# Kernel optimization log

Measured on AMD Instinct MI355X. Metric: run time of the kernel, lower is better.

The kernel has to match this reference:

```python
import jax, jax.numpy as jnp
import numpy as np
import math

N_FREQ = 128
D_EMB = 64
SLOT_DIM = 256
MLP_HIDDEN = 1024
B, N_SLOTS, N_FEAT = 32, 128, 4096
SIN_DIM = 1 + 2 * N_FREQ
EPS_LN = 1e-5


def _lin_init(key, dout, din):
    k1, k2 = jax.random.split(key)
    s = 1.0 / np.sqrt(din)
    w = jax.random.uniform(k1, (dout, din), minval=-s, maxval=s, dtype=jnp.float32)
    b = jax.random.uniform(k2, (dout,), minval=-s, maxval=s, dtype=jnp.float32)
    return w, b


def setup_inputs() -> dict:
    key = jax.random.key(0)
    ks = jax.random.split(key, 20)
    inp = {}
    # four TimeDepWeight heads: (prefix, d_out, d_in)
    heads = [("q", SLOT_DIM, SLOT_DIM), ("g", SLOT_DIM, 2 * SLOT_DIM),
             ("f0", MLP_HIDDEN, 2 * SLOT_DIM), ("f1", SLOT_DIM, MLP_HIDDEN)]
    i = 0
    for name, dout, din in heads:
        w0, b0 = _lin_init(ks[i], D_EMB, SIN_DIM)
        w1, b1 = _lin_init(ks[i + 1], D_EMB, D_EMB)
        wp, bp = _lin_init(ks[i + 2], dout * din, D_EMB)
        i += 3
        inp[f"{name}_w0"], inp[f"{name}_b0"] = w0, b0
        inp[f"{name}_w1"], inp[f"{name}_b1"] = w1, b1
        inp[f"{name}_wp"], inp[f"{name}_bp"] = wp, bp
    # LayerNorm affine params (eqx.nn.LayerNorm defaults: weight=1, bias=0)
    inp["lnA_w"] = jnp.ones((SLOT_DIM,), jnp.float32)
    inp["lnA_b"] = jnp.zeros((SLOT_DIM,), jnp.float32)
    inp["lnF_w"] = jnp.ones((SLOT_DIM,), jnp.float32)
    inp["lnF_b"] = jnp.zeros((SLOT_DIM,), jnp.float32)
    inp["t"] = jax.random.uniform(ks[12], (1,), dtype=jnp.float32)
    inp["slots"] = jax.random.normal(ks[13], (B, N_SLOTS, SLOT_DIM), jnp.float32)
    inp["k"] = jax.random.normal(ks[14], (B, N_FEAT, SLOT_DIM), jnp.float32)
    inp["v"] = jax.random.normal(ks[15], (B, N_FEAT, SLOT_DIM), jnp.float32)
    return inp


def _tdw(t, w0, b0, w1, b1, wp, bp, d_out, d_in):
    # Sinusoidal(t) -> 2-layer SiLU MLP -> proj -> [d_out, d_in]
    freqs = (-math.log(10000.0) / N_FREQ) * jnp.arange(N_FREQ, dtype=jnp.float32)
    wt = freqs * t
    emb = jnp.concatenate([t[None], jnp.sin(wt), jnp.cos(wt)])
    h = jax.nn.silu(w0 @ emb + b0)
    h = jax.nn.silu(w1 @ h + b1)
    return (wp @ h + bp).reshape(d_out, d_in)


def _layernorm(x, w, b):
    mu = x.mean(-1, keepdims=True)
    var = ((x - mu) ** 2).mean(-1, keepdims=True)
    return (x - mu) / jnp.sqrt(var + EPS_LN) * w + b


def reference(t, slots, k, v,
              q_w0, q_b0, q_w1, q_b1, q_wp, q_bp,
              g_w0, g_b0, g_w1, g_b1, g_wp, g_bp,
              f0_w0, f0_b0, f0_w1, f0_b1, f0_wp, f0_bp,
              f1_w0, f1_b0, f1_w1, f1_b1, f1_wp, f1_bp,
              lnA_w, lnA_b, lnF_w, lnF_b):
    ts = t[0]
    scale = SLOT_DIM ** (-0.5)
    W_q = _tdw(ts, q_w0, q_b0, q_w1, q_b1, q_wp, q_bp, SLOT_DIM, SLOT_DIM)
    W_gate = _tdw(ts, g_w0, g_b0, g_w1, g_b1, g_wp, g_bp, SLOT_DIM, 2 * SLOT_DIM)
    W_ff0 = _tdw(ts, f0_w0, f0_b0, f0_w1, f0_b1, f0_wp, f0_bp, MLP_HIDDEN, 2 * SLOT_DIM)
    W_ff1 = _tdw(ts, f1_w0, f1_b0, f1_w1, f1_b1, f1_wp, f1_bp, SLOT_DIM, MLP_HIDDEN)

    slots_norm = _layernorm(slots, lnA_w, lnA_b)                  # [B,N,D]
    q = jnp.einsum('bnd,od->bno', slots_norm, W_q)                # [B,N,D]
    att_logits = jnp.einsum('bnd,bmd->bnm', q, k) * scale         # [B,N,M]
    att = jax.nn.softmax(att_logits, axis=1)                      # over slots
    att = att / (att.sum(axis=-1, keepdims=True) + 1e-08)         # renorm over feats
    f_attn = jnp.einsum('bnm,bmd->bnd', att, v)                   # [B,N,D]

    gate_input = jnp.concatenate([slots_norm, f_attn], axis=-1)   # [B,N,2D]
    gate = jax.nn.sigmoid(jnp.einsum('bnd,od->bno', gate_input, W_gate))

    slots_ff = _layernorm(slots, lnF_w, lnF_b)
    ff_input = jnp.concatenate([slots_ff, f_attn], axis=-1)       # [B,N,2D]
    h = jax.nn.relu(jnp.einsum('bnd,od->bno', ff_input, W_ff0))   # [B,N,H]
    g_ff = jnp.einsum('bnd,od->bno', h, W_ff1)                    # [B,N,D]
    return gate * f_attn + g_ff
```

## Files before the change

### kernel.cpp

```cpp
#include <hip/hip_runtime.h>
#include <hip/hip_bf16.h>
#include <cstdint>

typedef unsigned short u16;
typedef unsigned int u32;
typedef __attribute__((ext_vector_type(8))) short short8;
typedef __attribute__((ext_vector_type(4))) float f32x4;

#define TID ((int)threadIdx.x)

__device__ __forceinline__ float b2f(u16 u) { return __uint_as_float(((u32)u) << 16); }
__device__ __forceinline__ u16 f2b(float f) {
    u32 u = __float_as_uint(f);
    u += 0x7fffu + ((u >> 16) & 1u);
    return (u16)(u >> 16);
}
__device__ __forceinline__ float2 upk(u32 u) {
    float2 r;
    r.x = __uint_as_float(u << 16);
    r.y = __uint_as_float(u & 0xffff0000u);
    return r;
}
__device__ __forceinline__ float silu_f(float x) { return x / (1.f + __expf(-x)); }

__device__ __forceinline__ float ldx(const void* p, size_t i, bool bf) {
    float v;
    if (bf) v = b2f(((const u16*)p)[i]);
    else    v = ((const float*)p)[i];
    return v;
}

#define BB 32
#define NN 128
#define DD 256
#define MM 4096
#define HH 1024
#define BN (BB * NN)

#define O_FLAG 0
#define O_H2   8
#define O_S    (O_H2 + 256)
#define O_FAT  (O_S + BN)
#define O_WQT  (O_FAT + BN * DD)
#define O_WGT  (O_WQT + 256 * 256)
#define O_WF0T (O_WGT + 512 * 256)
#define O_WF1T (O_WF0T + 512 * 1024)
#define O_SNA  (O_WF1T + 1024 * 256)
#define O_SNF  (O_SNA + BN * DD)
#define O_Q    (O_SNF + BN * DD)
#define O_H    (O_Q + BN * DD)
#define O_FATP O_H

__global__ void probe_dtype(const void* lnAw, int* flag) {
    u32 bits = *(const u32*)lnAw;
    *flag = ((bits & 0xFFFFu) == 0x3F80u) ? 1 : 0;
}

__global__ __launch_bounds__(256) void tdw_mlp(
    const void* t,
    const void* qw0, const void* qb0, const void* qw1, const void* qb1,
    const void* gw0, const void* gb0, const void* gw1, const void* gb1,
    const void* f0w0, const void* f0b0, const void* f0w1, const void* f0b1,
    const void* f1w0, const void* f1b0, const void* f1w1, const void* f1b1,
    float* h2out, const int* flagp)
{
    __shared__ float emb[257];
    __shared__ float h1s[256];
    bool bf = (*flagp != 0);
    float tv = ldx(t, 0, bf);
    const float c = -9.210340371976184f / 128.f;
    for (int i = TID; i < 257; i += 256) {
        float val;
        if (i == 0) val = tv;
        else if (i <= 128) val = sinf(c * (float)(i - 1) * tv);
        else val = cosf(c * (float)(i - 129) * tv);
        emb[i] = val;
    }
    __syncthreads();
    int head = TID >> 6, o = TID & 63;
    const void* w0s[4] = {qw0, gw0, f0w0, f1w0};
    const void* b0s[4] = {qb0, gb0, f0b0, f1b0};
    const void* w1s[4] = {qw1, gw1, f0w1, f1w1};
    const void* b1s[4] = {qb1, gb1, f0b1, f1b1};
    float acc = ldx(b0s[head], o, bf);
    if (bf) {
        const u16* w0 = (const u16*)w0s[head];
        for (int j = 0; j < 257; j++) acc += b2f(w0[o * 257 + j]) * emb[j];
    } else {
        const float* w0 = (const float*)w0s[head];
        for (int j = 0; j < 257; j++) acc += w0[o * 257 + j] * emb[j];
    }
    h1s[TID] = silu_f(acc);
    __syncthreads();
    float acc2 = ldx(b1s[head], o, bf);
    if (bf) {
        const u16* w1 = (const u16*)w1s[head];
        for (int j = 0; j < 64; j++) acc2 += b2f(w1[o * 64 + j]) * h1s[head * 64 + j];
    } else {
        const float* w1 = (const float*)w1s[head];
        for (int j = 0; j < 64; j++) acc2 += w1[o * 64 + j] * h1s[head * 64 + j];
    }
    h2out[TID] = silu_f(acc2);
}

__global__ __launch_bounds__(256) void tdw_proj(
    const void* __restrict__ wp, const void* __restrict__ bp,
    const float* __restrict__ h2, float* __restrict__ WT,
    int dout_shift, int din, const int* flagp)
{
    __shared__ float h2s[64];
    bool bf = (*flagp != 0);
    if (TID < 64) h2s[TID] = h2[TID];
    __syncthreads();
    int j = blockIdx.x * 256 + TID;
    int d = j >> dout_shift;
    int o = j & ((1 << dout_shift) - 1);
    long i = (long)o * din + d;
    float acc;
    if (bf) acc = b2f(((const u16*)bp)[i]);
    else    acc = ((const float*)bp)[i];
    if (bf) {
        const uint4* row = (const uint4*)((const u16*)wp + i * 64);
#pragma unroll
        for (int r = 0; r < 8; r++) {
            uint4 u = row[r];
            float2 p;
            p = upk(u.x); acc += p.x * h2s[r * 8 + 0] + p.y * h2s[r * 8 + 1];
            p = upk(u.y); acc += p.x * h2s[r * 8 + 2] + p.y * h2s[r * 8 + 3];
            p = upk(u.z); acc += p.x * h2s[r * 8 + 4] + p.y * h2s[r * 8 + 5];
            p = upk(u.w); acc += p.x * h2s[r * 8 + 6] + p.y * h2s[r * 8 + 7];
        }
    } else {
        const float4* row = (const float4*)((const float*)wp + i * 64);
#pragma unroll
        for (int r = 0; r < 16; r++) {
            float4 u = row[r];
            acc += u.x * h2s[r * 4 + 0] + u.y * h2s[r * 4 + 1]
                 + u.z * h2s[r * 4 + 2] + u.w * h2s[r * 4 + 3];
        }
    }
    WT[j] = acc;
}

__global__ __launch_bounds__(256) void layernorm_k(
    const void* __restrict__ slots,
    const void* lnAw, const void* lnAb, const void* lnFw, const void* lnFb,
    float* __restrict__ snA, float* __restrict__ snF, const int* flagp)
{
    int bn = blockIdx.x;
    bool bf = (*flagp != 0);
    float x;
    if (bf) x = b2f(((const u16*)slots)[(size_t)bn * DD + TID]);
    else    x = ((const float*)slots)[(size_t)bn * DD + TID];
    float s1 = x, s2 = x * x;
    for (int off = 32; off; off >>= 1) {
        s1 += __shfl_down(s1, off, 64);
        s2 += __shfl_down(s2, off, 64);
    }
    __shared__ float r1[4], r2[4];
    __shared__ float mu_s, rs_s;
    if ((TID & 63) == 0) { r1[TID >> 6] = s1; r2[TID >> 6] = s2; }
    __syncthreads();
    if (TID == 0) {
        float a = r1[0] + r1[1] + r1[2] + r1[3];
        float b = r2[0] + r2[1] + r2[2] + r2[3];
        float mu = a * (1.f / 256.f);
        float var = b * (1.f / 256.f) - mu * mu;
        mu_s = mu;
        rs_s = rsqrtf(var + 1e-5f);
    }
    __syncthreads();
    float xh = (x - mu_s) * rs_s;
    snA[(size_t)bn * DD + TID] = xh * ldx(lnAw, TID, bf) + ldx(lnAb, TID, bf);
    snF[(size_t)bn * DD + TID] = xh * ldx(lnFw, TID, bf) + ldx(lnFb, TID, bf);
}

__global__ __launch_bounds__(256) void qproj(
    const float* __restrict__ snA, const float* __restrict__ WqT, u16* __restrict__ qb)
{
    int rb = blockIdx.x;
    __shared__ float sn[8][256];
    for (int idx = TID; idx < 512; idx += 256) {
        int r = idx >> 6, q4 = idx & 63;
        *(float4*)&sn[r][q4 * 4] = *(const float4*)(snA + (size_t)rb * 2048 + r * 256 + q4 * 4);
    }
    __syncthreads();
    float acc[8] = {0, 0, 0, 0, 0, 0, 0, 0};
    for (int d = 0; d < 256; d += 4) {
        float w0 = WqT[(d + 0) * 256 + TID];
        float w1 = WqT[(d + 1) * 256 + TID];
        float w2 = WqT[(d + 2) * 256 + TID];
        float w3 = WqT[(d + 3) * 256 + TID];
#pragma unroll
        for (int r = 0; r < 8; r++) {
            float4 s4 = *(const float4*)&sn[r][d];
            acc[r] = fmaf(s4.x, w0, fmaf(s4.y, w1, fmaf(s4.z, w2, fmaf(s4.w, w3, acc[r]))));
        }
    }
    for (int r = 0; r < 8; r++) qb[(size_t)(rb * 8 + r) * 256 + TID] = f2b(acc[r]);
}

__global__ __launch_bounds__(256, 2) void attn_mfma(
    const u16* __restrict__ qbG,
    const void* __restrict__ k, const void* __restrict__ v,
    float* __restrict__ fatP, float* __restrict__ S, const int* flagp)
{
    const int b = blockIdx.y;
    const int mt = blockIdx.x;
    const int m0 = mt * 128;
    const bool bf = (*flagp != 0);
    const int t = TID;
    const int l = t & 63, w = t >> 6;
    const int lg = l >> 4;
    const int ll = l & 15;

    __shared__ alignas(16) u16 AB[128 * 128];
    __shared__ alignas(16) u16 vt[256 * 40];

    u16* qb = AB;
    u16* kb = AB + 8192;

    f32x4 acc[2][8];
#pragma unroll
    for (int s = 0; s < 2; s++)
#pragma unroll
        for (int nt = 0; nt < 8; nt++) acc[s][nt] = {0.f, 0.f, 0.f, 0.f};

    for (int dc = 0; dc < 4; dc++) {
        {
            const u32* qg = (const u32*)qbG + (size_t)b * 128 * 128 + dc * 32;
#pragma unroll
            for (int i = 0; i < 16; i++) {
                int fid = i * 256 + t;
                int n = fid >> 5, dp = fid & 31;
                u32 val = qg[n * 128 + dp];
                *(u32*)((char*)qb + n * 128 + ((dp * 4) ^ ((n & 7) << 4))) = val;
            }
        }
        if (bf) {
            const u32* kg = (const u32*)k + ((size_t)(b * MM + m0)) * 128 + dc * 32;
#pragma unroll
            for (int i = 0; i < 16; i++) {
                int fid = i * 256 + t;
                int mm = fid >> 5, dp = fid & 31;
                u32 val = kg[(size_t)mm * 128 + dp];
                *(u32*)((char*)kb + mm * 128 + ((dp * 4) ^ ((mm & 7) << 4))) = val;
            }
        } else {
            const float4* kg = (const float4*)k + ((size_t)(b * MM + m0)) * 64 + dc * 16;
#pragma unroll
            for (int i = 0; i < 8; i++) {
                int fid = i * 256 + t;
                int mm = fid >> 4, q4 = fid & 15;
                float4 f = kg[(size_t)mm * 64 + q4];
                u32 p0 = ((u32)f2b(f.x)) | ((u32)f2b(f.y) << 16);
                u32 p1 = ((u32)f2b(f.z)) | ((u32)f2b(f.w) << 16);
                char* base = (char*)kb + mm * 128;
                *(u32*)(base + (((q4 * 8) + 0) ^ ((mm & 7) << 4))) = p0;
                *(u32*)(base + (((q4 * 8) + 4) ^ ((mm & 7) << 4))) = p1;
            }
        }
        __syncthreads();
#pragma unroll
        for (int ds = 0; ds < 2; ds++) {
            int doff = ds * 64 + lg * 16;
            short8 bfr[2];
#pragma unroll
            for (int s = 0; s < 2; s++) {
                int mm = w * 32 + s * 16 + ll;
                bfr[s] = *(const short8*)((char*)kb + mm * 128 + (doff ^ ((mm & 7) << 4)));
            }
#pragma unroll
            for (int nt = 0; nt < 8; nt++) {
                int n = nt * 16 + ll;
                short8 af = *(const short8*)((char*)qb + n * 128 + (doff ^ ((n & 7) << 4)));
                acc[0][nt] = __builtin_amdgcn_mfma_f32_16x16x32_bf16(af, bfr[0], acc[0][nt], 0, 0, 0);
                acc[1][nt] = __builtin_amdgcn_mfma_f32_16x16x32_bf16(af, bfr[1], acc[1][nt], 0, 0, 0);
            }
        }
        __syncthreads();
    }

    const float scale = 0.0625f;
#pragma unroll
    for (int s = 0; s < 2; s++) {
        float cm = -1e30f;
#pragma unroll
        for (int nt = 0; nt < 8; nt++)
#pragma unroll
            for (int r = 0; r < 4; r++) cm = fmaxf(cm, acc[s][nt][r]);
        cm = fmaxf(cm, __shfl_xor(cm, 16));
        cm = fmaxf(cm, __shfl_xor(cm, 32));
        float cs = 0.f;
#pragma unroll
        for (int nt = 0; nt < 8; nt++)
#pragma unroll
            for (int r = 0; r < 4; r++) {
                float ev = __expf((acc[s][nt][r] - cm) * scale);
                acc[s][nt][r] = ev;
                cs += ev;
            }
        cs += __shfl_xor(cs, 16);
        cs += __shfl_xor(cs, 32);
        float inv = 1.f / cs;
#pragma unroll
        for (int nt = 0; nt < 8; nt++)
#pragma unroll
            for (int r = 0; r < 4; r++) acc[s][nt][r] *= inv;
    }

    u16* att = AB;
#pragma unroll
    for (int s = 0; s < 2; s++)
#pragma unroll
        for (int nt = 0; nt < 8; nt++)
#pragma unroll
            for (int r = 0; r < 4; r++) {
                int n = nt * 16 + lg * 4 + r;
                int mw = w * 32 + s * 16 + ll;
                *(u16*)((char*)att + n * 256 + ((mw * 2) ^ ((n & 7) << 4))) = f2b(acc[s][nt][r]);
            }
#pragma unroll
    for (int nt = 0; nt < 8; nt++)
#pragma unroll
        for (int r = 0; r < 4; r++) {
            float vsum = acc[0][nt][r] + acc[1][nt][r];
            vsum += __shfl_xor(vsum, 1);
            vsum += __shfl_xor(vsum, 2);
            vsum += __shfl_xor(vsum, 4);
            vsum += __shfl_xor(vsum, 8);
            if (ll == 0) atomicAdd(S + b * NN + nt * 16 + lg * 4 + r, vsum);
        }

    f32x4 accp[8][4];
#pragma unroll
    for (int nt = 0; nt < 8; nt++)
#pragma unroll
        for (int dt = 0; dt < 4; dt++) accp[nt][dt] = {0.f, 0.f, 0.f, 0.f};

    for (int ms = 0; ms < 4; ms++) {
        if (bf) {
            const u32* vg = (const u32*)v + ((size_t)(b * MM + m0 + ms * 32)) * 128;
#pragma unroll
            for (int i = 0; i < 16; i++) {
                int fid = i * 256 + t;
                int mm = fid >> 7, du = fid & 127;
                u32 val = vg[(size_t)mm * 128 + du];
                vt[(du * 2 + 0) * 40 + mm] = (u16)(val & 0xffffu);
                vt[(du * 2 + 1) * 40 + mm] = (u16)(val >> 16);
            }
        } else {
            const float4* vg = (const float4*)v + ((size_t)(b * MM + m0 + ms * 32)) * 64;
#pragma unroll
            for (int i = 0; i < 8; i++) {
                int fid = i * 256 + t;
                int mm = fid >> 6, q4 = fid & 63;
                float4 f = vg[(size_t)mm * 64 + q4];
                vt[(q4 * 4 + 0) * 40 + mm] = f2b(f.x);
                vt[(q4 * 4 + 1) * 40 + mm] = f2b(f.y);
                vt[(q4 * 4 + 2) * 40 + mm] = f2b(f.z);
                vt[(q4 * 4 + 3) * 40 + mm] = f2b(f.w);
            }
        }
        __syncthreads();
        short8 bfr[4];
#pragma unroll
        for (int dt = 0; dt < 4; dt++) {
            int dv = w * 64 + dt * 16 + ll;
            bfr[dt] = *(const short8*)(vt + dv * 40 + lg * 8);
        }
#pragma unroll
        for (int nt = 0; nt < 8; nt++) {
            int n = nt * 16 + ll;
            short8 af = *(const short8*)((char*)att + n * 256 + ((ms * 64 + lg * 16) ^ ((n & 7) << 4)));
#pragma unroll
            for (int dt = 0; dt < 4; dt++)
                accp[nt][dt] = __builtin_amdgcn_mfma_f32_16x16x32_bf16(af, bfr[dt], accp[nt][dt], 0, 0, 0);
        }
        __syncthreads();
    }

    float* fp = fatP + ((size_t)mt * BN + (size_t)b * NN) * DD;
#pragma unroll
    for (int nt = 0; nt < 8; nt++)
#pragma unroll
        for (int dt = 0; dt < 4; dt++)
#pragma unroll
            for (int r = 0; r < 4; r++) {
                int n = nt * 16 + lg * 4 + r;
                int dv = w * 64 + dt * 16 + ll;
                fp[(size_t)n * DD + dv] = accp[nt][dt][r];
            }
}

__global__ __launch_bounds__(256) void reduce_fat(
    const float* __restrict__ fatP, float* __restrict__ fat)
{
    size_t i = ((size_t)blockIdx.x * 256 + TID) * 4;
    float4 a = *(const float4*)(fatP + i);
#pragma unroll
    for (int mt = 1; mt < 32; mt++) {
        float4 bb = *(const float4*)(fatP + (size_t)mt * (size_t)BN * DD + i);
        a.x += bb.x; a.y += bb.y; a.z += bb.z; a.w += bb.w;
    }
    *(float4*)(fat + i) = a;
}

__global__ __launch_bounds__(256) void ffa(
    const float* __restrict__ snF, const float* __restrict__ fat, const float* __restrict__ S,
    const float* __restrict__ Wf0T, float* __restrict__ h)
{
    int rb = blockIdx.x;
    __shared__ float fi[8][512];
    __shared__ float rsh[8];
    if (TID < 8) rsh[TID] = 1.f / (S[rb * 8 + TID] + 1e-8f);
    __syncthreads();
    for (int idx = TID; idx < 1024; idx += 256) {
        int r = idx >> 7, q4 = idx & 127;
        size_t bn = (size_t)rb * 8 + r;
        float4 val;
        if (q4 < 64) val = *(const float4*)(snF + bn * 256 + q4 * 4);
        else {
            val = *(const float4*)(fat + bn * 256 + (q4 - 64) * 4);
            float s = rsh[r];
            val.x *= s; val.y *= s; val.z *= s; val.w *= s;
        }
        *(float4*)&fi[r][q4 * 4] = val;
    }
    __syncthreads();
    float acc[8][4] = {};
    for (int d = 0; d < 512; d += 4) {
        float w[4][4];
#pragma unroll
        for (int kk2 = 0; kk2 < 4; kk2++) {
            const float* wp_ = Wf0T + (size_t)(d + kk2) * 1024 + TID;
            w[kk2][0] = wp_[0];   w[kk2][1] = wp_[256];
            w[kk2][2] = wp_[512]; w[kk2][3] = wp_[768];
        }
#pragma unroll
        for (int r = 0; r < 8; r++) {
            float4 f = *(const float4*)&fi[r][d];
            float fv[4] = {f.x, f.y, f.z, f.w};
#pragma unroll
            for (int kk2 = 0; kk2 < 4; kk2++)
#pragma unroll
                for (int c = 0; c < 4; c++)
                    acc[r][c] = fmaf(fv[kk2], w[kk2][c], acc[r][c]);
        }
    }
    for (int r = 0; r < 8; r++) {
        size_t base = (size_t)(rb * 8 + r) * 1024;
        h[base + TID] = fmaxf(acc[r][0], 0.f);
        h[base + TID + 256] = fmaxf(acc[r][1], 0.f);
        h[base + TID + 512] = fmaxf(acc[r][2], 0.f);
        h[base + TID + 768] = fmaxf(acc[r][3], 0.f);
    }
}

__global__ __launch_bounds__(256) void ffb(
    const float* __restrict__ snA, const float* __restrict__ fat, const float* __restrict__ S,
    const float* __restrict__ WgT, const float* __restrict__ Wf1T,
    const float* __restrict__ h, void* __restrict__ out, const int* flagp)
{
    int rb = blockIdx.x;
    bool bf = (*flagp != 0);
    __shared__ float gi[8][512];
    __shared__ float hs[8][1024];
    __shared__ float rsh[8];
    if (TID < 8) rsh[TID] = 1.f / (S[rb * 8 + TID] + 1e-8f);
    __syncthreads();
    for (int idx = TID; idx < 1024; idx += 256) {
        int r = idx >> 7, q4 = idx & 127;
        size_t bn = (size_t)rb * 8 + r;
        float4 val;
        if (q4 < 64) val = *(const float4*)(snA + bn * 256 + q4 * 4);
        else {
            val = *(const float4*)(fat + bn * 256 + (q4 - 64) * 4);
            float s = rsh[r];
            val.x *= s; val.y *= s; val.z *= s; val.w *= s;
        }
        *(float4*)&gi[r][q4 * 4] = val;
    }
    for (int idx = TID; idx < 2048; idx += 256) {
        int r = idx >> 8, q4 = idx & 255;
        *(float4*)&hs[r][q4 * 4] = *(const float4*)(h + (size_t)(rb * 8 + r) * 1024 + q4 * 4);
    }
    __syncthreads();
    float ag[8] = {0, 0, 0, 0, 0, 0, 0, 0};
    float af[8] = {0, 0, 0, 0, 0, 0, 0, 0};
    for (int d = 0; d < 512; d += 4) {
        float w0 = WgT[(d + 0) * 256 + TID];
        float w1 = WgT[(d + 1) * 256 + TID];
        float w2 = WgT[(d + 2) * 256 + TID];
        float w3 = WgT[(d + 3) * 256 + TID];
#pragma unroll
        for (int r = 0; r < 8; r++) {
            float4 g = *(const float4*)&gi[r][d];
            ag[r] = fmaf(g.x, w0, fmaf(g.y, w1, fmaf(g.z, w2, fmaf(g.w, w3, ag[r]))));
        }
    }
    for (int j = 0; j < 1024; j += 4) {
        float w0 = Wf1T[(j + 0) * 256 + TID];
        float w1 = Wf1T[(j + 1) * 256 + TID];
        float w2 = Wf1T[(j + 2) * 256 + TID];
        float w3 = Wf1T[(j + 3) * 256 + TID];
#pragma unroll
        for (int r = 0; r < 8; r++) {
            float4 hv = *(const float4*)&hs[r][j];
            af[r] = fmaf(hv.x, w0, fmaf(hv.y, w1, fmaf(hv.z, w2, fmaf(hv.w, w3, af[r]))));
        }
    }
    for (int r = 0; r < 8; r++) {
        int bn = rb * 8 + r;
        float fa = gi[r][256 + TID];
        float g = 1.f / (1.f + __expf(-ag[r]));
        float val = g * fa + af[r];
        if (bf) ((u16*)out)[(size_t)bn * 256 + TID] = f2b(val);
        else    ((float*)out)[(size_t)bn * 256 + TID] = val;
    }
}

extern "C" void kernel_launch(void* const* d_in, const int* in_sizes, int n_in,
                              void* d_out, int out_size, void* d_ws, size_t ws_size,
                              hipStream_t stream)
{
    const void* in[32];
    bool sig_order = (n_in >= 1 && in_sizes[0] == 1);
    for (int i = 0; i < 32; i++) {
        int j = sig_order ? ((i < 28) ? (i + 4) : (i - 28)) : i;
        in[i] = d_in[j];
    }

    const void* qw0 = in[0];  const void* qb0 = in[1];
    const void* qw1 = in[2];  const void* qb1 = in[3];
    const void* qwp = in[4];  const void* qbp = in[5];
    const void* gw0 = in[6];  const void* gb0 = in[7];
    const void* gw1 = in[8];  const void* gb1 = in[9];
    const void* gwp = in[10]; const void* gbp = in[11];
    const void* f0w0 = in[12]; const void* f0b0 = in[13];
    const void* f0w1 = in[14]; const void* f0b1 = in[15];
    const void* f0wp = in[16]; const void* f0bp = in[17];
    const void* f1w0 = in[18]; const void* f1b0 = in[19];
    const void* f1w1 = in[20]; const void* f1b1 = in[21];
    const void* f1wp = in[22]; const void* f1bp = in[23];
    const void* lnAw = in[24]; const void* lnAb = in[25];
    const void* lnFw = in[26]; const void* lnFb = in[27];
    const void* t    = in[28]; const void* slots = in[29];
    const void* kk   = in[30]; const void* vv   = in[31];

    float* F = (float*)d_ws;
    int* flagp = (int*)(F + O_FLAG);

    hipMemsetAsync(F + O_S, 0, (size_t)BN * sizeof(float), stream);

    probe_dtype<<<1, 1, 0, stream>>>(lnAw, flagp);

    tdw_mlp<<<1, 256, 0, stream>>>(t, qw0, qb0, qw1, qb1, gw0, gb0, gw1, gb1,
                                   f0w0, f0b0, f0w1, f0b1, f1w0, f1b0, f1w1, f1b1,
                                   F + O_H2, flagp);

    tdw_proj<<<256, 256, 0, stream>>>(qwp, qbp, F + O_H2 + 0, F + O_WQT, 8, 256, flagp);
    tdw_proj<<<512, 256, 0, stream>>>(gwp, gbp, F + O_H2 + 64, F + O_WGT, 8, 512, flagp);
    tdw_proj<<<2048, 256, 0, stream>>>(f0wp, f0bp, F + O_H2 + 128, F + O_WF0T, 10, 512, flagp);
    tdw_proj<<<1024, 256, 0, stream>>>(f1wp, f1bp, F + O_H2 + 192, F + O_WF1T, 8, 1024, flagp);

    layernorm_k<<<BN, 256, 0, stream>>>(slots, lnAw, lnAb, lnFw, lnFb,
                                        F + O_SNA, F + O_SNF, flagp);

    qproj<<<BN / 8, 256, 0, stream>>>(F + O_SNA, F + O_WQT, (u16*)(F + O_Q));

    attn_mfma<<<dim3(MM / 128, BB), 256, 0, stream>>>((const u16*)(F + O_Q), kk, vv,
                                                      F + O_FATP, F + O_S, flagp);

    reduce_fat<<<BN * DD / 1024, 256, 0, stream>>>(F + O_FATP, F + O_FAT);

    ffa<<<BN / 8, 256, 0, stream>>>(F + O_SNF, F + O_FAT, F + O_S, F + O_WF0T, F + O_H);

    ffb<<<BN / 8, 256, 0, stream>>>(F + O_SNA, F + O_FAT, F + O_S, F + O_WGT, F + O_WF1T,
                                    F + O_H, d_out, flagp);
}
```

Measured before the change: 1.012 ms.

## Process two feature sub-tiles per attention block and use per-wave staging

Each attention block now covers 256 features in two 128-feature sub-tiles and keeps the att·V accumulator across both, which halves the number of fp32 partial outputs that reduce_fat has to sum. Q fragments are read straight from global memory instead of being staged in shared memory. K and V tiles go into per-wave shared-memory regions, so most block-wide barriers can be dropped. The costs are fewer blocks (less parallelism), uncoalesced strided column loads for V, and repeated global reads of Q.

```diff
diff --git a/kernel.cpp b/kernel.cpp
--- a/kernel.cpp
+++ b/kernel.cpp
@@ -36,6 +36,7 @@
 #define MM 4096
 #define HH 1024
 #define BN (BB * NN)
+#define NMT 16
 
 #define O_FLAG 0
 #define O_H2   8
@@ -207,175 +208,171 @@
 {
     const int b = blockIdx.y;
     const int mt = blockIdx.x;
-    const int m0 = mt * 128;
     const bool bf = (*flagp != 0);
     const int t = TID;
     const int l = t & 63, w = t >> 6;
     const int lg = l >> 4;
     const int ll = l & 15;
 
-    __shared__ alignas(16) u16 AB[128 * 128];
-    __shared__ alignas(16) u16 vt[256 * 40];
-
-    u16* qb = AB;
-    u16* kb = AB + 8192;
-
-    f32x4 acc[2][8];
-#pragma unroll
-    for (int s = 0; s < 2; s++)
-#pragma unroll
-        for (int nt = 0; nt < 8; nt++) acc[s][nt] = {0.f, 0.f, 0.f, 0.f};
-
-    for (int dc = 0; dc < 4; dc++) {
-        {
-            const u32* qg = (const u32*)qbG + (size_t)b * 128 * 128 + dc * 32;
-#pragma unroll
-            for (int i = 0; i < 16; i++) {
-                int fid = i * 256 + t;
-                int n = fid >> 5, dp = fid & 31;
-                u32 val = qg[n * 128 + dp];
-                *(u32*)((char*)qb + n * 128 + ((dp * 4) ^ ((n & 7) << 4))) = val;
-            }
-        }
-        if (bf) {
-            const u32* kg = (const u32*)k + ((size_t)(b * MM + m0)) * 128 + dc * 32;
-#pragma unroll
-            for (int i = 0; i < 16; i++) {
-                int fid = i * 256 + t;
-                int mm = fid >> 5, dp = fid & 31;
-                u32 val = kg[(size_t)mm * 128 + dp];
-                *(u32*)((char*)kb + mm * 128 + ((dp * 4) ^ ((mm & 7) << 4))) = val;
-            }
-        } else {
-            const float4* kg = (const float4*)k + ((size_t)(b * MM + m0)) * 64 + dc * 16;
-#pragma unroll
-            for (int i = 0; i < 8; i++) {
-                int fid = i * 256 + t;
-                int mm = fid >> 4, q4 = fid & 15;
-                float4 f = kg[(size_t)mm * 64 + q4];
-                u32 p0 = ((u32)f2b(f.x)) | ((u32)f2b(f.y) << 16);
-                u32 p1 = ((u32)f2b(f.z)) | ((u32)f2b(f.w) << 16);
-                char* base = (char*)kb + mm * 128;
-                *(u32*)(base + (((q4 * 8) + 0) ^ ((mm & 7) << 4))) = p0;
-                *(u32*)(base + (((q4 * 8) + 4) ^ ((mm & 7) << 4))) = p1;
-            }
-        }
+    __shared__ alignas(16) u16 att[128 * 128];
+    __shared__ alignas(16) u16 vt[4 * 2176];
+
+    char* kb_w = (char*)att + w * 4096;
+    char* vt_w = (char*)vt + w * 4352;
+
+    const u16* qrow = qbG + (size_t)(b * 128) * 256;
+
+    f32x4 accp[8][4];
+#pragma unroll
+    for (int nt = 0; nt < 8; nt++)
+#pragma unroll
+        for (int dt = 0; dt < 4; dt++) accp[nt][dt] = {0.f, 0.f, 0.f, 0.f};
+
+    for (int sub = 0; sub < 2; sub++) {
+        const int msub = mt * 256 + sub * 128;
+
+        f32x4 acc[2][8];
+#pragma unroll
+        for (int s = 0; s < 2; s++)
+#pragma unroll
+            for (int nt = 0; nt < 8; nt++) acc[s][nt] = {0.f, 0.f, 0.f, 0.f};
+
+        for (int dc = 0; dc < 4; dc++) {
+            if (bf) {
+                const u32* kg = (const u32*)k + ((size_t)(b * MM + msub + w * 32)) * 128 + dc * 32;
+#pragma unroll
+                for (int i = 0; i < 16; i++) {
+                    int fid = i * 64 + l;
+                    int dp = fid & 31, lm = fid >> 5;
+                    u32 val = kg[(size_t)lm * 128 + dp];
+                    *(u32*)(kb_w + lm * 128 + ((dp * 4) ^ ((lm & 7) << 4))) = val;
+                }
+            } else {
+                const float2* kg = (const float2*)k + ((size_t)(b * MM + msub + w * 32)) * 128 + dc * 32;
+#pragma unroll
+                for (int i = 0; i < 16; i++) {
+                    int fid = i * 64 + l;
+                    int dp = fid & 31, lm = fid >> 5;
+                    float2 f = kg[(size_t)lm * 128 + dp];
+                    u32 val = (u32)f2b(f.x) | ((u32)f2b(f.y) << 16);
+                    *(u32*)(kb_w + lm * 128 + ((dp * 4) ^ ((lm & 7) << 4))) = val;
+                }
+            }
+            asm volatile("" ::: "memory");
+#pragma unroll
+            for (int ds = 0; ds < 2; ds++) {
+                int doff = ds * 64 + lg * 16;
+                short8 bfr[2];
+#pragma unroll
+                for (int s = 0; s < 2; s++) {
+                    int lm = s * 16 + ll;
+                    bfr[s] = *(const short8*)(kb_w + lm * 128 + (doff ^ ((lm & 7) << 4)));
+                }
+#pragma unroll
+                for (int nt = 0; nt < 8; nt++) {
+                    short8 af = *(const short8*)(qrow + (size_t)(nt * 16 + ll) * 256
+                                                 + dc * 64 + ds * 32 + lg * 8);
+                    acc[0][nt] = __builtin_amdgcn_mfma_f32_16x16x32_bf16(af, bfr[0], acc[0][nt], 0, 0, 0);
+                    acc[1][nt] = __builtin_amdgcn_mfma_f32_16x16x32_bf16(af, bfr[1], acc[1][nt], 0, 0, 0);
+                }
+            }
+            asm volatile("" ::: "memory");
+        }
+
+        const float scale = 0.0625f;
+#pragma unroll
+        for (int s = 0; s < 2; s++) {
+            float cm = -1e30f;
+#pragma unroll
+            for (int nt = 0; nt < 8; nt++)
+#pragma unroll
+                for (int r = 0; r < 4; r++) cm = fmaxf(cm, acc[s][nt][r]);
+            cm = fmaxf(cm, __shfl_xor(cm, 16));
+            cm = fmaxf(cm, __shfl_xor(cm, 32));
+            float cs = 0.f;
+#pragma unroll
+            for (int nt = 0; nt < 8; nt++)
+#pragma unroll
+                for (int r = 0; r < 4; r++) {
+                    float ev = __expf((acc[s][nt][r] - cm) * scale);
+                    acc[s][nt][r] = ev;
+                    cs += ev;
+                }
+            cs += __shfl_xor(cs, 16);
+            cs += __shfl_xor(cs, 32);
+            float inv = 1.f / cs;
+#pragma unroll
+            for (int nt = 0; nt < 8; nt++)
+#pragma unroll
+                for (int r = 0; r < 4; r++) acc[s][nt][r] *= inv;
+        }
+
         __syncthreads();
-#pragma unroll
-        for (int ds = 0; ds < 2; ds++) {
-            int doff = ds * 64 + lg * 16;
-            short8 bfr[2];
-#pragma unroll
-            for (int s = 0; s < 2; s++) {
-                int mm = w * 32 + s * 16 + ll;
-                bfr[s] = *(const short8*)((char*)kb + mm * 128 + (doff ^ ((mm & 7) << 4)));
+
+#pragma unroll
+        for (int s = 0; s < 2; s++)
+#pragma unroll
+            for (int nt = 0; nt < 8; nt++)
+#pragma unroll
+                for (int r = 0; r < 4; r++) {
+                    int n = nt * 16 + lg * 4 + r;
+                    int mw = w * 32 + s * 16 + ll;
+                    *(u16*)((char*)att + n * 256 + ((mw * 2) ^ ((n & 7) << 4))) = f2b(acc[s][nt][r]);
+                }
+#pragma unroll
+        for (int nt = 0; nt < 8; nt++)
+#pragma unroll
+            for (int r = 0; r < 4; r++) {
+                float vsum = acc[0][nt][r] + acc[1][nt][r];
+                vsum += __shfl_xor(vsum, 1);
+                vsum += __shfl_xor(vsum, 2);
+                vsum += __shfl_xor(vsum, 4);
+                vsum += __shfl_xor(vsum, 8);
+                if (ll == 0) atomicAdd(S + b * NN + nt * 16 + lg * 4 + r, vsum);
+            }
+        __syncthreads();
+
+        for (int ms = 0; ms < 4; ms++) {
+            if (bf) {
+                const u16* vg = (const u16*)v + ((size_t)(b * MM + msub + ms * 32)) * 256 + w * 64 + l;
+                u16 tmp[32];
+#pragma unroll
+                for (int mm = 0; mm < 32; mm++) tmp[mm] = vg[(size_t)mm * 256];
+#pragma unroll
+                for (int m2 = 0; m2 < 16; m2++)
+                    *(u32*)(vt_w + l * 68 + m2 * 4) = (u32)tmp[2 * m2] | ((u32)tmp[2 * m2 + 1] << 16);
+            } else {
+                const float* vg = (const float*)v + ((size_t)(b * MM + msub + ms * 32)) * 256 + w * 64 + l;
+                u16 tmp[32];
+#pragma unroll
+                for (int mm = 0; mm < 32; mm++) tmp[mm] = f2b(vg[(size_t)mm * 256]);
+#pragma unroll
+                for (int m2 = 0; m2 < 16; m2++)
+                    *(u32*)(vt_w + l * 68 + m2 * 4) = (u32)tmp[2 * m2] | ((u32)tmp[2 * m2 + 1] << 16);
+            }
+            asm volatile("" ::: "memory");
+            union U8 { short8 s8; u32 u[4]; };
+            short8 bfr[4];
+#pragma unroll
+            for (int dt = 0; dt < 4; dt++) {
+                const char* vb = vt_w + (dt * 16 + ll) * 68 + lg * 16;
+                U8 bu;
+                bu.u[0] = *(const u32*)(vb + 0);
+                bu.u[1] = *(const u32*)(vb + 4);
+                bu.u[2] = *(const u32*)(vb + 8);
+                bu.u[3] = *(const u32*)(vb + 12);
+                bfr[dt] = bu.s8;
             }
 #pragma unroll
             for (int nt = 0; nt < 8; nt++) {
                 int n = nt * 16 + ll;
-                short8 af = *(const short8*)((char*)qb + n * 128 + (doff ^ ((n & 7) << 4)));
-                acc[0][nt] = __builtin_amdgcn_mfma_f32_16x16x32_bf16(af, bfr[0], acc[0][nt], 0, 0, 0);
-                acc[1][nt] = __builtin_amdgcn_mfma_f32_16x16x32_bf16(af, bfr[1], acc[1][nt], 0, 0, 0);
-            }
-        }
-        __syncthreads();
-    }
-
-    const float scale = 0.0625f;
-#pragma unroll
-    for (int s = 0; s < 2; s++) {
-        float cm = -1e30f;
-#pragma unroll
-        for (int nt = 0; nt < 8; nt++)
-#pragma unroll
-            for (int r = 0; r < 4; r++) cm = fmaxf(cm, acc[s][nt][r]);
-        cm = fmaxf(cm, __shfl_xor(cm, 16));
-        cm = fmaxf(cm, __shfl_xor(cm, 32));
-        float cs = 0.f;
-#pragma unroll
-        for (int nt = 0; nt < 8; nt++)
-#pragma unroll
-            for (int r = 0; r < 4; r++) {
-                float ev = __expf((acc[s][nt][r] - cm) * scale);
-                acc[s][nt][r] = ev;
-                cs += ev;
-            }
-        cs += __shfl_xor(cs, 16);
-        cs += __shfl_xor(cs, 32);
-        float inv = 1.f / cs;
-#pragma unroll
-        for (int nt = 0; nt < 8; nt++)
-#pragma unroll
-            for (int r = 0; r < 4; r++) acc[s][nt][r] *= inv;
-    }
-
-    u16* att = AB;
-#pragma unroll
-    for (int s = 0; s < 2; s++)
-#pragma unroll
-        for (int nt = 0; nt < 8; nt++)
-#pragma unroll
-            for (int r = 0; r < 4; r++) {
-                int n = nt * 16 + lg * 4 + r;
-                int mw = w * 32 + s * 16 + ll;
-                *(u16*)((char*)att + n * 256 + ((mw * 2) ^ ((n & 7) << 4))) = f2b(acc[s][nt][r]);
-            }
-#pragma unroll
-    for (int nt = 0; nt < 8; nt++)
-#pragma unroll
-        for (int r = 0; r < 4; r++) {
-            float vsum = acc[0][nt][r] + acc[1][nt][r];
-            vsum += __shfl_xor(vsum, 1);
-            vsum += __shfl_xor(vsum, 2);
-            vsum += __shfl_xor(vsum, 4);
-            vsum += __shfl_xor(vsum, 8);
-            if (ll == 0) atomicAdd(S + b * NN + nt * 16 + lg * 4 + r, vsum);
-        }
-
-    f32x4 accp[8][4];
-#pragma unroll
-    for (int nt = 0; nt < 8; nt++)
-#pragma unroll
-        for (int dt = 0; dt < 4; dt++) accp[nt][dt] = {0.f, 0.f, 0.f, 0.f};
-
-    for (int ms = 0; ms < 4; ms++) {
-        if (bf) {
-            const u32* vg = (const u32*)v + ((size_t)(b * MM + m0 + ms * 32)) * 128;
-#pragma unroll
-            for (int i = 0; i < 16; i++) {
-                int fid = i * 256 + t;
-                int mm = fid >> 7, du = fid & 127;
-                u32 val = vg[(size_t)mm * 128 + du];
-                vt[(du * 2 + 0) * 40 + mm] = (u16)(val & 0xffffu);
-                vt[(du * 2 + 1) * 40 + mm] = (u16)(val >> 16);
-            }
-        } else {
-            const float4* vg = (const float4*)v + ((size_t)(b * MM + m0 + ms * 32)) * 64;
-#pragma unroll
-            for (int i = 0; i < 8; i++) {
-                int fid = i * 256 + t;
-                int mm = fid >> 6, q4 = fid & 63;
-                float4 f = vg[(size_t)mm * 64 + q4];
-                vt[(q4 * 4 + 0) * 40 + mm] = f2b(f.x);
-                vt[(q4 * 4 + 1) * 40 + mm] = f2b(f.y);
-                vt[(q4 * 4 + 2) * 40 + mm] = f2b(f.z);
-                vt[(q4 * 4 + 3) * 40 + mm] = f2b(f.w);
-            }
-        }
-        __syncthreads();
-        short8 bfr[4];
-#pragma unroll
-        for (int dt = 0; dt < 4; dt++) {
-            int dv = w * 64 + dt * 16 + ll;
-            bfr[dt] = *(const short8*)(vt + dv * 40 + lg * 8);
-        }
-#pragma unroll
-        for (int nt = 0; nt < 8; nt++) {
-            int n = nt * 16 + ll;
-            short8 af = *(const short8*)((char*)att + n * 256 + ((ms * 64 + lg * 16) ^ ((n & 7) << 4)));
-#pragma unroll
-            for (int dt = 0; dt < 4; dt++)
-                accp[nt][dt] = __builtin_amdgcn_mfma_f32_16x16x32_bf16(af, bfr[dt], accp[nt][dt], 0, 0, 0);
+                short8 af = *(const short8*)((char*)att + n * 256
+                                             + ((ms * 64 + lg * 16) ^ ((n & 7) << 4)));
+#pragma unroll
+                for (int dt = 0; dt < 4; dt++)
+                    accp[nt][dt] = __builtin_amdgcn_mfma_f32_16x16x32_bf16(af, bfr[dt], accp[nt][dt], 0, 0, 0);
+            }
+            asm volatile("" ::: "memory");
         }
         __syncthreads();
     }
@@ -399,7 +396,7 @@
     size_t i = ((size_t)blockIdx.x * 256 + TID) * 4;
     float4 a = *(const float4*)(fatP + i);
 #pragma unroll
-    for (int mt = 1; mt < 32; mt++) {
+    for (int mt = 1; mt < NMT; mt++) {
         float4 bb = *(const float4*)(fatP + (size_t)mt * (size_t)BN * DD + i);
         a.x += bb.x; a.y += bb.y; a.z += bb.z; a.w += bb.w;
     }
@@ -569,7 +566,7 @@
 
     qproj<<<BN / 8, 256, 0, stream>>>(F + O_SNA, F + O_WQT, (u16*)(F + O_Q));
 
-    attn_mfma<<<dim3(MM / 128, BB), 256, 0, stream>>>((const u16*)(F + O_Q), kk, vv,
+    attn_mfma<<<dim3(MM / 256, BB), 256, 0, stream>>>((const u16*)(F + O_Q), kk, vv,
                                                       F + O_FATP, F + O_S, flagp);
 
     reduce_fat<<<BN * DD / 1024, 256, 0, stream>>>(F + O_FATP, F + O_FAT);
```

Result: slower. 1.047 ms (+3.5%).
